# Optimization experiments

Measured on AMD Instinct MI355X. Metric: run time of the kernel, lower is better.

## Reference

```python
import jax, jax.numpy as jnp
import numpy as np

B, A, H1, H2 = 128, 64, 256, 256


def setup_inputs() -> dict:
    key = jax.random.key(0)
    k1, k2, k3, k4, k5, k6 = jax.random.split(key, 6)
    scale = 0.01
    return {
        "userAspRep": jax.random.normal(k1, (B, A, H1), dtype=jnp.float32),
        "itemAspRep": jax.random.normal(k2, (B, A, H1), dtype=jnp.float32),
        "W_u": jax.random.uniform(k3, (H2, H1), jnp.float32, -scale, scale),
        "W_i": jax.random.uniform(k4, (H2, H1), jnp.float32, -scale, scale),
        "w_hu": jax.random.uniform(k5, (H2, 1), jnp.float32, -scale, scale),
        "w_hi": jax.random.uniform(k6, (H2, 1), jnp.float32, -scale, scale),
    }


def reference(userAspRep, itemAspRep, W_u, W_i, w_hu, w_hi):
    # L1 pairwise similarity: sim[b,u,i] = 1 / (1 + sum_h |U[b,u,h] - I[b,i,h]|)
    diff = jnp.abs(userAspRep[:, :, None, :] - itemAspRep[:, None, :, :])  # [B,Au,Ai,H1]
    sim = 1.0 / (1.0 + diff.sum(axis=-1))  # [B,Au,Ai]

    Wu_u = jnp.einsum('kh,buh->bku', W_u, userAspRep)  # [B,H2,Au]
    Wi_i = jnp.einsum('kh,bih->bki', W_i, itemAspRep)  # [B,H2,Ai]

    # User aspect importance
    H_u = jax.nn.relu(Wu_u + jnp.einsum('bki,bui->bku', Wi_i, sim))  # [B,H2,Au]
    user_scores = jnp.einsum('k,bku->bu', w_hu[:, 0], H_u)  # [B,Au]
    userAspImpt = jax.nn.softmax(user_scores, axis=1)

    # Item aspect importance
    H_i = jax.nn.relu(Wi_i + jnp.einsum('bku,bui->bki', Wu_u, sim))  # [B,H2,Ai]
    item_scores = jnp.einsum('k,bki->bi', w_hi[:, 0], H_i)  # [B,Ai]
    itemAspImpt = jax.nn.softmax(item_scores, axis=1)

    return (userAspImpt, itemAspImpt)
```

## Files before the change

kernel.cpp:

```cpp
#include <hip/hip_runtime.h>

#define NB 128
#define NA 64
#define NH1 256
#define NH2 256

typedef __attribute__((ext_vector_type(8))) short bf16x8;
typedef __attribute__((ext_vector_type(4))) float f32x4;
typedef __attribute__((ext_vector_type(8))) unsigned short u16x8;
typedef __attribute__((ext_vector_type(4))) unsigned short u16x4;

__device__ __forceinline__ unsigned short f2bf(float f) {
    union { float f; unsigned u; } v; v.f = f;
    unsigned r = v.u + 0x7FFFu + ((v.u >> 16) & 1u);
    return (unsigned short)(r >> 16);
}

__global__ __launch_bounds__(256) void cvt_w(
    const float* __restrict__ Wu, const float* __restrict__ Wi,
    unsigned short* __restrict__ Wub, unsigned short* __restrict__ Wib)
{
    const size_t e = ((size_t)blockIdx.x * 256 + threadIdx.x) * 8;
    const float* src; unsigned short* dst; size_t off;
    if (e < 65536) { src = Wu; dst = Wub; off = e; }
    else           { src = Wi; dst = Wib; off = e - 65536; }
    float4 a = *reinterpret_cast<const float4*>(src + off);
    float4 b = *reinterpret_cast<const float4*>(src + off + 4);
    u16x8 o;
    o[0] = f2bf(a.x); o[1] = f2bf(a.y); o[2] = f2bf(a.z); o[3] = f2bf(a.w);
    o[4] = f2bf(b.x); o[5] = f2bf(b.y); o[6] = f2bf(b.z); o[7] = f2bf(b.w);
    *reinterpret_cast<u16x8*>(dst + off) = o;
}

#define SPAD 260
__global__ __launch_bounds__(256) void sim_kernel(
    const float* __restrict__ U, const float* __restrict__ I,
    unsigned short* __restrict__ SIM, unsigned short* __restrict__ SIMT)
{
    __shared__ float Ush[32 * SPAD];
    __shared__ float Ish[64 * SPAD];
    const int t = threadIdx.x, b = blockIdx.x, uh = blockIdx.y;

    const float4* Ug = reinterpret_cast<const float4*>(U + ((size_t)b * NA + uh * 32) * NH1);
    const float4* Ig = reinterpret_cast<const float4*>(I + (size_t)b * NA * NH1);
    #pragma unroll
    for (int k = 0; k < 24; ++k) {
        const int g = t + k * 256;
        if (k < 8) {
            float4 v = Ug[g];
            *reinterpret_cast<float4*>(&Ush[(g >> 6) * SPAD + (g & 63) * 4]) = v;
        } else {
            const int g2 = g - 2048;
            float4 v = Ig[g2];
            *reinterpret_cast<float4*>(&Ish[(g2 >> 6) * SPAD + (g2 & 63) * 4]) = v;
        }
    }
    __syncthreads();

    const int tx = t & 15, ty = t >> 4;
    float acc[2][4] = {};
    #pragma unroll 4
    for (int h4 = 0; h4 < 64; ++h4) {
        float4 uv[2], iv[4];
        uv[0] = *reinterpret_cast<const float4*>(&Ush[ty * SPAD + h4 * 4]);
        uv[1] = *reinterpret_cast<const float4*>(&Ush[(ty + 16) * SPAD + h4 * 4]);
        #pragma unroll
        for (int di = 0; di < 4; ++di)
            iv[di] = *reinterpret_cast<const float4*>(&Ish[(tx + di * 16) * SPAD + h4 * 4]);
        #pragma unroll
        for (int du = 0; du < 2; ++du)
            #pragma unroll
            for (int di = 0; di < 4; ++di)
                acc[du][di] += fabsf(uv[du].x - iv[di].x) + fabsf(uv[du].y - iv[di].y)
                             + fabsf(uv[du].z - iv[di].z) + fabsf(uv[du].w - iv[di].w);
    }

    unsigned short* SB = SIM  + (size_t)b * NA * NA;
    unsigned short* TB = SIMT + (size_t)b * NA * NA;
    #pragma unroll
    for (int du = 0; du < 2; ++du) {
        const int u = uh * 32 + ty + du * 16;
        #pragma unroll
        for (int di = 0; di < 4; ++di) {
            const int i = tx + di * 16;
            const unsigned short sv = f2bf(1.0f / (1.0f + acc[du][di]));
            SB[(size_t)u * NA + i] = sv;
            TB[(size_t)i * NA + u] = sv;
        }
    }
}

#define XPAD 264
#define PPAD 72
__global__ __launch_bounds__(1024) void fused_kernel(
    const float* __restrict__ U, const float* __restrict__ I,
    const unsigned short* __restrict__ Wub, const unsigned short* __restrict__ Wib,
    const unsigned short* __restrict__ SIM, const unsigned short* __restrict__ SIMT,
    const float* __restrict__ whu, const float* __restrict__ whi,
    float* __restrict__ out)
{
    __shared__ unsigned short Xl[2][64 * XPAD];
    __shared__ unsigned short Pl[2][256 * PPAD];
    __shared__ float red[16 * 64];
    const int t = threadIdx.x, b = blockIdx.x;

    #pragma unroll
    for (int k = 0; k < 8; ++k) {
        const int g = t + k * 1024;
        const int side = g >> 12;
        const int rem = g & 4095;
        const float* X = side ? I : U;
        float4 v = *reinterpret_cast<const float4*>(
            X + ((size_t)b * NA + (rem >> 6)) * NH1 + (rem & 63) * 4);
        u16x4 o;
        o[0] = f2bf(v.x); o[1] = f2bf(v.y); o[2] = f2bf(v.z); o[3] = f2bf(v.w);
        *reinterpret_cast<u16x4*>(&Xl[side][(rem >> 6) * XPAD + (rem & 63) * 4]) = o;
    }
    __syncthreads();

    const int w  = __builtin_amdgcn_readfirstlane(t >> 6);
    const int l  = t & 63;
    const int lr = l & 15;
    const int lk = (l >> 4) * 8;
    const int s  = w >> 3;
    const int wk = w & 7;

    const unsigned short* Wb = s ? Wib : Wub;
    f32x4 acc[2][4];
    #pragma unroll
    for (int kt = 0; kt < 2; ++kt)
        #pragma unroll
        for (int at = 0; at < 4; ++at) acc[kt][at] = (f32x4)(0.f);

    #pragma unroll
    for (int h0 = 0; h0 < NH1; h0 += 32) {
        bf16x8 afr[2], bfr[4];
        #pragma unroll
        for (int kt = 0; kt < 2; ++kt)
            afr[kt] = *reinterpret_cast<const bf16x8*>(
                Wb + (size_t)(wk * 32 + kt * 16 + lr) * NH1 + h0 + lk);
        #pragma unroll
        for (int at = 0; at < 4; ++at)
            bfr[at] = *reinterpret_cast<const bf16x8*>(
                &Xl[s][(at * 16 + lr) * XPAD + h0 + lk]);
        #pragma unroll
        for (int kt = 0; kt < 2; ++kt)
            #pragma unroll
            for (int at = 0; at < 4; ++at)
                acc[kt][at] = __builtin_amdgcn_mfma_f32_16x16x32_bf16(
                    afr[kt], bfr[at], acc[kt][at], 0, 0, 0);
    }

    #pragma unroll
    for (int kt = 0; kt < 2; ++kt) {
        const int kb = wk * 32 + kt * 16 + (l >> 4) * 4;
        #pragma unroll
        for (int at = 0; at < 4; ++at)
            #pragma unroll
            for (int r = 0; r < 4; ++r)
                Pl[s][(kb + r) * PPAD + at * 16 + lr] = f2bf(acc[kt][at][r]);
    }
    __syncthreads();

    const unsigned short* SMg = (s ? SIMT : SIM) + (size_t)b * NA * NA;
    const unsigned short* Alds = Pl[s ^ 1];
    const float* wv = s ? whi : whu;

    float partial[4] = {0.f, 0.f, 0.f, 0.f};
    #pragma unroll
    for (int kt = 0; kt < 2; ++kt) {
        f32x4 sacc[4];
        #pragma unroll
        for (int ot = 0; ot < 4; ++ot) sacc[ot] = (f32x4)(0.f);
        #pragma unroll
        for (int kk = 0; kk < NA; kk += 32) {
            bf16x8 af = *reinterpret_cast<const bf16x8*>(
                &Alds[(wk * 32 + kt * 16 + lr) * PPAD + kk + lk]);
            #pragma unroll
            for (int ot = 0; ot < 4; ++ot) {
                bf16x8 bf = *reinterpret_cast<const bf16x8*>(
                    SMg + (size_t)(ot * 16 + lr) * NA + kk + lk);
                sacc[ot] = __builtin_amdgcn_mfma_f32_16x16x32_bf16(af, bf, sacc[ot], 0, 0, 0);
            }
        }
        const int kb = wk * 32 + kt * 16 + (l >> 4) * 4;
        float wreg[4];
        #pragma unroll
        for (int r = 0; r < 4; ++r) wreg[r] = wv[kb + r];
        #pragma unroll
        for (int ot = 0; ot < 4; ++ot) {
            float p = 0.f;
            #pragma unroll
            for (int r = 0; r < 4; ++r) {
                float h = acc[kt][ot][r] + sacc[ot][r];
                h = fmaxf(h, 0.f);
                p = fmaf(wreg[r], h, p);
            }
            partial[ot] += p;
        }
    }
    #pragma unroll
    for (int ot = 0; ot < 4; ++ot) {
        partial[ot] += __shfl_xor(partial[ot], 16, 64);
        partial[ot] += __shfl_xor(partial[ot], 32, 64);
    }
    if (l < 16) {
        #pragma unroll
        for (int ot = 0; ot < 4; ++ot) red[w * 64 + ot * 16 + l] = partial[ot];
    }
    __syncthreads();

    if (t < 128) {
        const int side = t >> 6, own = t & 63;
        float sc = 0.f;
        #pragma unroll
        for (int q = 0; q < 8; ++q) sc += red[(side * 8 + q) * 64 + own];
        float m = sc;
        #pragma unroll
        for (int off = 32; off >= 1; off >>= 1) m = fmaxf(m, __shfl_xor(m, off, 64));
        float e = __expf(sc - m);
        float ssum = e;
        #pragma unroll
        for (int off = 32; off >= 1; off >>= 1) ssum += __shfl_xor(ssum, off, 64);
        out[(size_t)side * (NB * NA) + (size_t)b * NA + own] = e / ssum;
    }
}

extern "C" void kernel_launch(void* const* d_in, const int* in_sizes, int n_in,
                              void* d_out, int out_size, void* d_ws, size_t ws_size,
                              hipStream_t stream)
{
    const float* U   = (const float*)d_in[0];
    const float* I   = (const float*)d_in[1];
    const float* Wu  = (const float*)d_in[2];
    const float* Wi  = (const float*)d_in[3];
    const float* whu = (const float*)d_in[4];
    const float* whi = (const float*)d_in[5];
    float* out = (float*)d_out;

    char* ws = (char*)d_ws;
    unsigned short* Wub  = (unsigned short*)(ws);
    unsigned short* Wib  = (unsigned short*)(ws + 131072);
    unsigned short* SIMb = (unsigned short*)(ws + 262144);
    unsigned short* SIMTb= (unsigned short*)(ws + 1310720);

    cvt_w<<<64, 256, 0, stream>>>(Wu, Wi, Wub, Wib);
    sim_kernel<<<dim3(NB, 2), 256, 0, stream>>>(U, I, SIMb, SIMTb);
    fused_kernel<<<NB, 1024, 0, stream>>>(U, I, Wub, Wib, SIMb, SIMTb, whu, whi, out);
}
```

Measured before the change: 104.6 us.

## Use packed fp16 L1 distance, split fused kernel per side, swizzle LDS

The similarity kernel now stores inputs in shared memory as fp16 and accumulates absolute differences with packed half2 arithmetic across 512 threads, each owning one user row. The fused kernel is split into a 2D grid with one block per batch and side. Each block recomputes both projections (its own side and the other side) so the two blocks need no cross-block exchange. LDS layouts use XOR swizzling instead of padding, and the similarity fragments are preloaded into registers. This trades duplicated projection MFMA work and fp16 accumulation accuracy over 256 terms for more parallel blocks and cheaper distance arithmetic.

Result: faster. 94.96 us (-9.2%).

```diff
diff --git a/kernel.cpp b/kernel.cpp
--- a/kernel.cpp
+++ b/kernel.cpp
@@ -9,12 +9,18 @@
 typedef __attribute__((ext_vector_type(4))) float f32x4;
 typedef __attribute__((ext_vector_type(8))) unsigned short u16x8;
 typedef __attribute__((ext_vector_type(4))) unsigned short u16x4;
+typedef _Float16 f16x2 __attribute__((ext_vector_type(2)));
 
 __device__ __forceinline__ unsigned short f2bf(float f) {
     union { float f; unsigned u; } v; v.f = f;
     unsigned r = v.u + 0x7FFFu + ((v.u >> 16) & 1u);
     return (unsigned short)(r >> 16);
 }
+__device__ __forceinline__ f16x2 habs2(f16x2 x) {
+    union { f16x2 h; unsigned u; } v; v.h = x; v.u &= 0x7FFF7FFFu; return v.h;
+}
+
+#define XSWZ(row, cb) ((cb) ^ (((row) & 7) << 4))
 
 __global__ __launch_bounds__(256) void cvt_w(
     const float* __restrict__ Wu, const float* __restrict__ Wi,
@@ -32,89 +38,83 @@
     *reinterpret_cast<u16x8*>(dst + off) = o;
 }
 
-#define SPAD 260
-__global__ __launch_bounds__(256) void sim_kernel(
+#define SROW 264
+__global__ __launch_bounds__(512) void sim_kernel(
     const float* __restrict__ U, const float* __restrict__ I,
     unsigned short* __restrict__ SIM, unsigned short* __restrict__ SIMT)
 {
-    __shared__ float Ush[32 * SPAD];
-    __shared__ float Ish[64 * SPAD];
+    __shared__ __align__(16) _Float16 sh[96 * SROW];
     const int t = threadIdx.x, b = blockIdx.x, uh = blockIdx.y;
 
     const float4* Ug = reinterpret_cast<const float4*>(U + ((size_t)b * NA + uh * 32) * NH1);
     const float4* Ig = reinterpret_cast<const float4*>(I + (size_t)b * NA * NH1);
     #pragma unroll
-    for (int k = 0; k < 24; ++k) {
-        const int g = t + k * 256;
-        if (k < 8) {
-            float4 v = Ug[g];
-            *reinterpret_cast<float4*>(&Ush[(g >> 6) * SPAD + (g & 63) * 4]) = v;
-        } else {
-            const int g2 = g - 2048;
-            float4 v = Ig[g2];
-            *reinterpret_cast<float4*>(&Ish[(g2 >> 6) * SPAD + (g2 & 63) * 4]) = v;
-        }
+    for (int it = 0; it < 12; ++it) {
+        const int g = t + it * 512;
+        float4 v = (g < 2048) ? Ug[g] : Ig[g - 2048];
+        const int row = g >> 6, c4 = g & 63;
+        f16x2 h0; h0.x = (_Float16)v.x; h0.y = (_Float16)v.y;
+        f16x2 h1; h1.x = (_Float16)v.z; h1.y = (_Float16)v.w;
+        union { f16x2 h[2]; float2 f; } pk; pk.h[0] = h0; pk.h[1] = h1;
+        *reinterpret_cast<float2*>(&sh[row * SROW + c4 * 4]) = pk.f;
     }
     __syncthreads();
 
     const int tx = t & 15, ty = t >> 4;
-    float acc[2][4] = {};
+    f16x2 acc[4];
+    #pragma unroll
+    for (int di = 0; di < 4; ++di) { acc[di].x = (_Float16)0; acc[di].y = (_Float16)0; }
+
+    const _Float16* Urow = &sh[ty * SROW];
     #pragma unroll 4
-    for (int h4 = 0; h4 < 64; ++h4) {
-        float4 uv[2], iv[4];
-        uv[0] = *reinterpret_cast<const float4*>(&Ush[ty * SPAD + h4 * 4]);
-        uv[1] = *reinterpret_cast<const float4*>(&Ush[(ty + 16) * SPAD + h4 * 4]);
-        #pragma unroll
-        for (int di = 0; di < 4; ++di)
-            iv[di] = *reinterpret_cast<const float4*>(&Ish[(tx + di * 16) * SPAD + h4 * 4]);
-        #pragma unroll
-        for (int du = 0; du < 2; ++du)
-            #pragma unroll
-            for (int di = 0; di < 4; ++di)
-                acc[du][di] += fabsf(uv[du].x - iv[di].x) + fabsf(uv[du].y - iv[di].y)
-                             + fabsf(uv[du].z - iv[di].z) + fabsf(uv[du].w - iv[di].w);
-    }
-
+    for (int h8 = 0; h8 < 32; ++h8) {
+        union { float4 f; f16x2 h[4]; } uv, iv;
+        uv.f = *reinterpret_cast<const float4*>(&Urow[h8 * 8]);
+        #pragma unroll
+        for (int di = 0; di < 4; ++di) {
+            iv.f = *reinterpret_cast<const float4*>(&sh[(32 + tx + di * 16) * SROW + h8 * 8]);
+            #pragma unroll
+            for (int c = 0; c < 4; ++c)
+                acc[di] = acc[di] + habs2(uv.h[c] - iv.h[c]);
+        }
+    }
+
+    const int u = uh * 32 + ty;
     unsigned short* SB = SIM  + (size_t)b * NA * NA;
     unsigned short* TB = SIMT + (size_t)b * NA * NA;
     #pragma unroll
-    for (int du = 0; du < 2; ++du) {
-        const int u = uh * 32 + ty + du * 16;
-        #pragma unroll
-        for (int di = 0; di < 4; ++di) {
-            const int i = tx + di * 16;
-            const unsigned short sv = f2bf(1.0f / (1.0f + acc[du][di]));
-            SB[(size_t)u * NA + i] = sv;
-            TB[(size_t)i * NA + u] = sv;
-        }
-    }
-}
-
-#define XPAD 264
-#define PPAD 72
-__global__ __launch_bounds__(1024) void fused_kernel(
+    for (int di = 0; di < 4; ++di) {
+        const int i = tx + di * 16;
+        const float sum = (float)acc[di].x + (float)acc[di].y;
+        const unsigned short sv = f2bf(1.0f / (1.0f + sum));
+        SB[(size_t)u * NA + i] = sv;
+        TB[(size_t)i * NA + u] = sv;
+    }
+}
+
+__global__ __launch_bounds__(512) void fused_kernel(
     const float* __restrict__ U, const float* __restrict__ I,
     const unsigned short* __restrict__ Wub, const unsigned short* __restrict__ Wib,
     const unsigned short* __restrict__ SIM, const unsigned short* __restrict__ SIMT,
     const float* __restrict__ whu, const float* __restrict__ whi,
     float* __restrict__ out)
 {
-    __shared__ unsigned short Xl[2][64 * XPAD];
-    __shared__ unsigned short Pl[2][256 * PPAD];
-    __shared__ float red[16 * 64];
-    const int t = threadIdx.x, b = blockIdx.x;
-
-    #pragma unroll
-    for (int k = 0; k < 8; ++k) {
-        const int g = t + k * 1024;
-        const int side = g >> 12;
-        const int rem = g & 4095;
+    __shared__ __align__(16) unsigned short Xl[2 * 64 * 256];
+    __shared__ __align__(16) unsigned short Pl[256 * 64];
+    __shared__ float red[8 * 64];
+    const int t = threadIdx.x, b = blockIdx.x, s = blockIdx.y;
+
+    #pragma unroll
+    for (int it = 0; it < 16; ++it) {
+        const int g = t + it * 512;
+        const int side = g >> 12, rem = g & 4095;
+        const int row = rem >> 6, c4 = rem & 63;
         const float* X = side ? I : U;
-        float4 v = *reinterpret_cast<const float4*>(
-            X + ((size_t)b * NA + (rem >> 6)) * NH1 + (rem & 63) * 4);
+        float4 v = *reinterpret_cast<const float4*>(X + ((size_t)b * NA + row) * NH1 + c4 * 4);
         u16x4 o;
         o[0] = f2bf(v.x); o[1] = f2bf(v.y); o[2] = f2bf(v.z); o[3] = f2bf(v.w);
-        *reinterpret_cast<u16x4*>(&Xl[side][(rem >> 6) * XPAD + (rem & 63) * 4]) = o;
+        char* dst = (char*)Xl + side * 32768 + row * 512 + XSWZ(row, c4 * 8);
+        *reinterpret_cast<u16x4*>(dst) = o;
     }
     __syncthreads();
 
@@ -122,49 +122,65 @@
     const int l  = t & 63;
     const int lr = l & 15;
     const int lk = (l >> 4) * 8;
-    const int s  = w >> 3;
-    const int wk = w & 7;
-
-    const unsigned short* Wb = s ? Wib : Wub;
-    f32x4 acc[2][4];
+
+    const unsigned short* Ws = s ? Wib : Wub;
+    const unsigned short* Wo = s ? Wub : Wib;
+
+    f32x4 accO[2][4], accX[2][4];
     #pragma unroll
     for (int kt = 0; kt < 2; ++kt)
         #pragma unroll
-        for (int at = 0; at < 4; ++at) acc[kt][at] = (f32x4)(0.f);
+        for (int at = 0; at < 4; ++at) { accO[kt][at] = (f32x4)(0.f); accX[kt][at] = (f32x4)(0.f); }
 
     #pragma unroll
     for (int h0 = 0; h0 < NH1; h0 += 32) {
-        bf16x8 afr[2], bfr[4];
+        bf16x8 as_[2], ao_[2], bs_[4], bo_[4];
+        #pragma unroll
+        for (int kt = 0; kt < 2; ++kt) {
+            const size_t roff = (size_t)(w * 32 + kt * 16 + lr) * NH1 + h0 + lk;
+            as_[kt] = *reinterpret_cast<const bf16x8*>(Ws + roff);
+            ao_[kt] = *reinterpret_cast<const bf16x8*>(Wo + roff);
+        }
+        #pragma unroll
+        for (int at = 0; at < 4; ++at) {
+            const int row = at * 16 + lr;
+            const int cb  = XSWZ(row, (h0 + lk) * 2);
+            bs_[at] = *reinterpret_cast<const bf16x8*>((char*)Xl + s * 32768 + row * 512 + cb);
+            bo_[at] = *reinterpret_cast<const bf16x8*>((char*)Xl + (s ^ 1) * 32768 + row * 512 + cb);
+        }
         #pragma unroll
         for (int kt = 0; kt < 2; ++kt)
-            afr[kt] = *reinterpret_cast<const bf16x8*>(
-                Wb + (size_t)(wk * 32 + kt * 16 + lr) * NH1 + h0 + lk);
+            #pragma unroll
+            for (int at = 0; at < 4; ++at) {
+                accO[kt][at] = __builtin_amdgcn_mfma_f32_16x16x32_bf16(as_[kt], bs_[at], accO[kt][at], 0, 0, 0);
+                accX[kt][at] = __builtin_amdgcn_mfma_f32_16x16x32_bf16(ao_[kt], bo_[at], accX[kt][at], 0, 0, 0);
+            }
+    }
+
+    #pragma unroll
+    for (int kt = 0; kt < 2; ++kt) {
+        const int kb = w * 32 + kt * 16 + (l >> 4) * 4;
         #pragma unroll
         for (int at = 0; at < 4; ++at)
-            bfr[at] = *reinterpret_cast<const bf16x8*>(
-                &Xl[s][(at * 16 + lr) * XPAD + h0 + lk]);
-        #pragma unroll
-        for (int kt = 0; kt < 2; ++kt)
-            #pragma unroll
-            for (int at = 0; at < 4; ++at)
-                acc[kt][at] = __builtin_amdgcn_mfma_f32_16x16x32_bf16(
-                    afr[kt], bfr[at], acc[kt][at], 0, 0, 0);
-    }
-
-    #pragma unroll
-    for (int kt = 0; kt < 2; ++kt) {
-        const int kb = wk * 32 + kt * 16 + (l >> 4) * 4;
-        #pragma unroll
-        for (int at = 0; at < 4; ++at)
-            #pragma unroll
-            for (int r = 0; r < 4; ++r)
-                Pl[s][(kb + r) * PPAD + at * 16 + lr] = f2bf(acc[kt][at][r]);
+            #pragma unroll
+            for (int r = 0; r < 4; ++r) {
+                const int row = kb + r;
+                *reinterpret_cast<unsigned short*>(
+                    (char*)Pl + row * 128 + XSWZ(row, (at * 16 + lr) * 2)) = f2bf(accX[kt][at][r]);
+            }
     }
     __syncthreads();
 
     const unsigned short* SMg = (s ? SIMT : SIM) + (size_t)b * NA * NA;
-    const unsigned short* Alds = Pl[s ^ 1];
     const float* wv = s ? whi : whu;
+
+    bf16x8 bfr2[2][4];
+    #pragma unroll
+    for (int kk2 = 0; kk2 < 2; ++kk2)
+        #pragma unroll
+        for (int ot = 0; ot < 4; ++ot)
+            bfr2[kk2][ot] = *reinterpret_cast<const bf16x8*>(
+                SMg + (size_t)(ot * 16 + lr) * NA + kk2 * 32 + lk);
 
     float partial[4] = {0.f, 0.f, 0.f, 0.f};
     #pragma unroll
@@ -173,28 +189,26 @@
         #pragma unroll
         for (int ot = 0; ot < 4; ++ot) sacc[ot] = (f32x4)(0.f);
         #pragma unroll
-        for (int kk = 0; kk < NA; kk += 32) {
+        for (int kk2 = 0; kk2 < 2; ++kk2) {
+            const int arow = w * 32 + kt * 16 + lr;
             bf16x8 af = *reinterpret_cast<const bf16x8*>(
-                &Alds[(wk * 32 + kt * 16 + lr) * PPAD + kk + lk]);
-            #pragma unroll
-            for (int ot = 0; ot < 4; ++ot) {
-                bf16x8 bf = *reinterpret_cast<const bf16x8*>(
-                    SMg + (size_t)(ot * 16 + lr) * NA + kk + lk);
-                sacc[ot] = __builtin_amdgcn_mfma_f32_16x16x32_bf16(af, bf, sacc[ot], 0, 0, 0);
-            }
-        }
-        const int kb = wk * 32 + kt * 16 + (l >> 4) * 4;
-        float wreg[4];
-        #pragma unroll
-        for (int r = 0; r < 4; ++r) wreg[r] = wv[kb + r];
+                (char*)Pl + arow * 128 + XSWZ(arow, (kk2 * 32 + lk) * 2));
+            #pragma unroll
+            for (int ot = 0; ot < 4; ++ot)
+                sacc[ot] = __builtin_amdgcn_mfma_f32_16x16x32_bf16(af, bfr2[kk2][ot], sacc[ot], 0, 0, 0);
+        }
+        const int kb = w * 32 + kt * 16 + (l >> 4) * 4;
+        float wr[4];
+        #pragma unroll
+        for (int r = 0; r < 4; ++r) wr[r] = wv[kb + r];
         #pragma unroll
         for (int ot = 0; ot < 4; ++ot) {
             float p = 0.f;
             #pragma unroll
             for (int r = 0; r < 4; ++r) {
-                float h = acc[kt][ot][r] + sacc[ot][r];
+                float h = accO[kt][ot][r] + sacc[ot][r];
                 h = fmaxf(h, 0.f);
-                p = fmaf(wreg[r], h, p);
+                p = fmaf(wr[r], h, p);
             }
             partial[ot] += p;
         }
@@ -210,11 +224,10 @@
     }
     __syncthreads();
 
-    if (t < 128) {
-        const int side = t >> 6, own = t & 63;
+    if (t < 64) {
         float sc = 0.f;
         #pragma unroll
-        for (int q = 0; q < 8; ++q) sc += red[(side * 8 + q) * 64 + own];
+        for (int q = 0; q < 8; ++q) sc += red[q * 64 + t];
         float m = sc;
         #pragma unroll
         for (int off = 32; off >= 1; off >>= 1) m = fmaxf(m, __shfl_xor(m, off, 64));
@@ -222,7 +235,7 @@
         float ssum = e;
         #pragma unroll
         for (int off = 32; off >= 1; off >>= 1) ssum += __shfl_xor(ssum, off, 64);
-        out[(size_t)side * (NB * NA) + (size_t)b * NA + own] = e / ssum;
+        out[(size_t)s * (NB * NA) + (size_t)b * NA + t] = e / ssum;
     }
 }
 
@@ -230,6 +243,7 @@
                               void* d_out, int out_size, void* d_ws, size_t ws_size,
                               hipStream_t stream)
 {
+    (void)in_sizes; (void)n_in; (void)out_size; (void)ws_size;
     const float* U   = (const float*)d_in[0];
     const float* I   = (const float*)d_in[1];
     const float* Wu  = (const float*)d_in[2];
@@ -239,12 +253,12 @@
     float* out = (float*)d_out;
 
     char* ws = (char*)d_ws;
-    unsigned short* Wub  = (unsigned short*)(ws);
-    unsigned short* Wib  = (unsigned short*)(ws + 131072);
-    unsigned short* SIMb = (unsigned short*)(ws + 262144);
-    unsigned short* SIMTb= (unsigned short*)(ws + 1310720);
+    unsigned short* Wub   = (unsigned short*)(ws);
+    unsigned short* Wib   = (unsigned short*)(ws + 131072);
+    unsigned short* SIMb  = (unsigned short*)(ws + 262144);
+    unsigned short* SIMTb = (unsigned short*)(ws + 1310720);
 
     cvt_w<<<64, 256, 0, stream>>>(Wu, Wi, Wub, Wib);
-    sim_kernel<<<dim3(NB, 2), 256, 0, stream>>>(U, I, SIMb, SIMTb);
-    fused_kernel<<<NB, 1024, 0, stream>>>(U, I, Wub, Wib, SIMb, SIMTb, whu, whi, out);
-}
+    sim_kernel<<<dim3(NB, 2), 512, 0, stream>>>(U, I, SIMb, SIMTb);
+    fused_kernel<<<dim3(NB, 2), 512, 0, stream>>>(U, I, Wub, Wib, SIMb, SIMTb, whu, whi, out);
+}
```
